# Kernel optimization log

Hardware: AMD Instinct MI355X
Metric: run time of the kernel (lower is better)

The kernel has to match this reference:

```python
import jax, jax.numpy as jnp
import numpy as np

B, L, H = 32, 1024, 512
NEG_INF = -1e30

def setup_inputs() -> dict:
    key = jax.random.key(0)
    k1, k2, k3, k4, k5 = jax.random.split(key, 5)
    c = jax.random.normal(k1, (B, L, H), dtype=jnp.float32)
    c_mask = jax.random.randint(k2, (B, L), 0, 2, dtype=jnp.int32)
    # xavier_uniform-like init scale for [H,1]: sqrt(6/(H+1))
    lim = float(np.sqrt(6.0 / (H + 1)))
    c_weight = jax.random.uniform(k3, (H, 1), minval=-lim, maxval=lim, dtype=jnp.float32)
    q_weight = jax.random.uniform(k4, (H, 1), minval=-lim, maxval=lim, dtype=jnp.float32)
    cq_weight = jax.random.uniform(k5, (1, 1, H), minval=-lim, maxval=lim, dtype=jnp.float32)
    bias = jnp.zeros((1,), dtype=jnp.float32)
    return {"c": c, "c_mask": c_mask, "c_weight": c_weight, "q_weight": q_weight,
            "cq_weight": cq_weight, "bias": bias}

def reference(c, c_mask, c_weight, q_weight, cq_weight, bias):
    m = c_mask.astype(jnp.float32)                     # [B,L]
    # similarity matrix (BiDAF trilinear decomposition), q == c here
    s0 = c @ c_weight                                  # [B,L,1]
    s1 = jnp.swapaxes(c @ q_weight, 1, 2)              # [B,1,L]
    s2 = jnp.einsum('blh,bmh->blm', c * cq_weight, c)  # [B,L,L]
    s = s0 + s1 + s2 + bias                            # [B,L,L]
    mask_row = m[:, None, :]                           # mask over dim=2 (keys)
    mask_col = m[:, :, None]                           # mask over dim=1
    s1p = jax.nn.softmax(mask_row * s + (1.0 - mask_row) * NEG_INF, axis=2)
    s2p = jax.nn.softmax(mask_col * s + (1.0 - mask_col) * NEG_INF, axis=1)
    a = s1p @ c                                        # [B,L,H]
    b = (s1p @ jnp.swapaxes(s2p, 1, 2)) @ c            # [B,L,H]
    return jnp.concatenate([c, a, c * a, c * b], axis=2)  # [B,L,4H]
```

## Files before the change

### kernel.cpp

```cpp
#include <hip/hip_runtime.h>
#include <hip/hip_bf16.h>
#include <stdint.h>

constexpr int Bb = 32;
constexpr int Ll = 1024;
constexpr int Hh = 512;

typedef __attribute__((ext_vector_type(8))) short short8;
typedef __attribute__((ext_vector_type(4))) short short4v;
typedef __attribute__((ext_vector_type(4))) float float4v;
typedef __attribute__((ext_vector_type(4))) int int4v;

__device__ inline short f2bf(float f) {
  union { float f; uint32_t u; } v; v.f = f;
  uint32_t r = (v.u + 0x7FFF + ((v.u >> 16) & 1)) >> 16;
  return (short)r;
}

#define MFMA(a, b, c) __builtin_amdgcn_mfma_f32_16x16x32_bf16(a, b, c, 0, 0, 0)

__device__ inline void gl_lds(const short* g, short* l) {
  __builtin_amdgcn_global_load_lds(
      (const __attribute__((address_space(1))) unsigned int*)g,
      (__attribute__((address_space(3))) unsigned int*)l, 16, 0, 0);
}

template <int ROWS>
__device__ inline void stage(short* lds, const short* g, int sk, int t) {
  const int w = t >> 6;
  const int kbg = (t & 7) ^ ((t >> 3) & 7);
#pragma unroll
  for (int r = 0; r < ROWS / 32; ++r) {
    int row = r * 32 + (t >> 3);
    gl_lds(g + (size_t)row * sk + kbg * 8, lds + (r * 32 + w * 8) * 64);
  }
}

__device__ inline short8 fld(const short* lds, int row, int kb) {
  return *(const short8*)(lds + row * 64 + ((kb ^ (row & 7)) << 3));
}

__global__ __launch_bounds__(256) void k_rowdots(
    const float* __restrict__ c, const float* __restrict__ cw,
    const float* __restrict__ qw, float* __restrict__ s0, float* __restrict__ s1) {
  int row = blockIdx.x * 4 + (threadIdx.x >> 6);
  int lane = threadIdx.x & 63;
  const float* cr = c + (size_t)row * Hh;
  float d0 = 0.f, d1 = 0.f;
#pragma unroll
  for (int i = 0; i < Hh / 64; ++i) {
    int h = lane + i * 64;
    float v = cr[h];
    d0 = fmaf(v, cw[h], d0);
    d1 = fmaf(v, qw[h], d1);
  }
#pragma unroll
  for (int off = 32; off > 0; off >>= 1) {
    d0 += __shfl_down(d0, off);
    d1 += __shfl_down(d1, off);
  }
  if (lane == 0) { s0[row] = d0; s1[row] = d1; }
}

__global__ __launch_bounds__(256) void k_cvt(
    const float* __restrict__ c, const float* __restrict__ cq,
    short* __restrict__ c16, short* __restrict__ cbq16) {
  size_t i8 = ((size_t)blockIdx.x * 256 + threadIdx.x) * 8;
  int h = (int)(i8 & (Hh - 1));
  float4v v0 = *(const float4v*)&c[i8];
  float4v v1 = *(const float4v*)&c[i8 + 4];
  float4v q0 = *(const float4v*)&cq[h];
  float4v q1 = *(const float4v*)&cq[h + 4];
  short8 a, bq;
#pragma unroll
  for (int j = 0; j < 4; ++j) {
    a[j] = f2bf(v0[j]);     a[4 + j] = f2bf(v1[j]);
    bq[j] = f2bf(v0[j] * q0[j]); bq[4 + j] = f2bf(v1[j] * q1[j]);
  }
  *(short8*)&c16[i8] = a;
  *(short8*)&cbq16[i8] = bq;
}

__global__ __launch_bounds__(256) void k_ct(const float* __restrict__ c,
                                            short* __restrict__ cT) {
  const int b = blockIdx.z, h0 = blockIdx.x * 64, l0 = blockIdx.y * 64;
  __shared__ short T[64 * 65];
  const int t = threadIdx.x, rl = t >> 4, c4 = (t & 15) * 4;
#pragma unroll
  for (int p = 0; p < 4; ++p) {
    int ll = rl + p * 16;
    float4v v = *(const float4v*)&c[((size_t)(b * Ll + l0 + ll)) * Hh + h0 + c4];
#pragma unroll
    for (int j = 0; j < 4; ++j) T[ll * 65 + c4 + j] = f2bf(v[j]);
  }
  __syncthreads();
#pragma unroll
  for (int p = 0; p < 4; ++p) {
    int hh = rl + p * 16;
    short4v o;
#pragma unroll
    for (int j = 0; j < 4; ++j) o[j] = T[(c4 + j) * 65 + hh];
    *(short4v*)&cT[((size_t)(b * Hh + h0 + hh)) * Ll + l0 + c4] = o;
  }
}

__global__ __launch_bounds__(256) void k_sgemm(
    const short* __restrict__ Aq, const short* __restrict__ Bc,
    const float* __restrict__ s0, const float* __restrict__ s1,
    const float* __restrict__ bias, float* __restrict__ S) {
  const int b = blockIdx.z, l0 = blockIdx.y * 128, m0 = blockIdx.x * 128;
  __shared__ __align__(16) short As[128 * 64];
  __shared__ __align__(16) short Bs[128 * 64];
  const int t = threadIdx.x, li = t & 63, w = t >> 6;
  const int wy = w >> 1, wx = w & 1, rr = li & 15, q = li >> 4;
  const short* Ag = Aq + ((size_t)b * Ll + l0) * Hh;
  const short* Bg = Bc + ((size_t)b * Ll + m0) * Hh;
  float4v acc[4][4];
#pragma unroll
  for (int i = 0; i < 4; ++i)
#pragma unroll
    for (int j = 0; j < 4; ++j) acc[i][j] = (float4v){0.f, 0.f, 0.f, 0.f};
  for (int kk = 0; kk < Hh; kk += 64) {
    stage<128>(As, Ag + kk, Hh, t);
    stage<128>(Bs, Bg + kk, Hh, t);
    __syncthreads();
#pragma unroll
    for (int ks = 0; ks < 2; ++ks) {
      int kb = ks * 4 + q;
      short8 af[4], bf4[4];
#pragma unroll
      for (int mt = 0; mt < 4; ++mt) af[mt] = fld(As, wy * 64 + mt * 16 + rr, kb);
#pragma unroll
      for (int nt = 0; nt < 4; ++nt) bf4[nt] = fld(Bs, wx * 64 + nt * 16 + rr, kb);
#pragma unroll
      for (int mt = 0; mt < 4; ++mt)
#pragma unroll
        for (int nt = 0; nt < 4; ++nt)
          acc[mt][nt] = MFMA(af[mt], bf4[nt], acc[mt][nt]);
    }
    __syncthreads();
  }
  const float bsc = bias[0];
  float* Sb = S + (size_t)b * Ll * Ll;
#pragma unroll
  for (int nt = 0; nt < 4; ++nt) {
    int m = m0 + wx * 64 + nt * 16 + rr;
    float s1v = s1[b * Ll + m] + bsc;
#pragma unroll
    for (int mt = 0; mt < 4; ++mt) {
#pragma unroll
      for (int i = 0; i < 4; ++i) {
        int l = l0 + wy * 64 + mt * 16 + q * 4 + i;
        Sb[(size_t)l * Ll + m] = acc[mt][nt][i] + s0[b * Ll + l] + s1v;
      }
    }
  }
}

__global__ __launch_bounds__(256) void k_rowstats(
    const float* __restrict__ S, const int* __restrict__ c_mask,
    float* __restrict__ rowmax, float* __restrict__ rowrcp) {
  int row = blockIdx.x * 4 + (threadIdx.x >> 6);
  int b = row >> 10;
  int lane = threadIdx.x & 63;
  const float* Sr = S + (size_t)row * Ll;
  const int* mk = c_mask + b * Ll;
  float vals[16];
  float mx = -INFINITY;
#pragma unroll
  for (int i = 0; i < 16; ++i) {
    int m = lane + i * 64;
    float v = mk[m] ? Sr[m] : -INFINITY;
    vals[i] = v;
    mx = fmaxf(mx, v);
  }
#pragma unroll
  for (int off = 32; off > 0; off >>= 1) mx = fmaxf(mx, __shfl_down(mx, off));
  mx = __shfl(mx, 0);
  float sum = 0.f;
#pragma unroll
  for (int i = 0; i < 16; ++i) sum += __expf(vals[i] - mx);
#pragma unroll
  for (int off = 32; off > 0; off >>= 1) sum += __shfl_down(sum, off);
  if (lane == 0) { rowmax[row] = mx; rowrcp[row] = 1.f / sum; }
}

__global__ __launch_bounds__(256) void k_colpart(
    const float* __restrict__ S, const int* __restrict__ c_mask,
    float* __restrict__ pmax, float* __restrict__ psum) {
  int b = blockIdx.z, l0 = blockIdx.y * 128;
  int m = blockIdx.x * 256 + threadIdx.x;
  const float* Sb = S + (size_t)b * Ll * Ll;
  const int* mk = c_mask + b * Ll;
  float mx = -INFINITY;
  for (int l = l0; l < l0 + 128; ++l)
    if (mk[l]) mx = fmaxf(mx, Sb[(size_t)l * Ll + m]);
  float sum = 0.f;
  if (mx > -INFINITY)
    for (int l = l0; l < l0 + 128; ++l)
      if (mk[l]) sum += __expf(Sb[(size_t)l * Ll + m] - mx);
  int o = blockIdx.y * (Bb * Ll) + b * Ll + m;
  pmax[o] = mx;
  psum[o] = sum;
}

__global__ __launch_bounds__(256) void k_colcomb(
    const float* __restrict__ pmax, const float* __restrict__ psum,
    float* __restrict__ colmax, float* __restrict__ colrcp) {
  int i = blockIdx.x * 256 + threadIdx.x;
  float M = -INFINITY;
#pragma unroll
  for (int k = 0; k < 8; ++k) M = fmaxf(M, pmax[k * (Bb * Ll) + i]);
  float s = 0.f;
#pragma unroll
  for (int k = 0; k < 8; ++k) {
    float pm = pmax[k * (Bb * Ll) + i];
    if (pm > -INFINITY) s += psum[k * (Bb * Ll) + i] * __expf(pm - M);
  }
  colmax[i] = M;
  colrcp[i] = 1.f / s;
}

__global__ __launch_bounds__(256) void k_p1(
    const float* __restrict__ S, const int* __restrict__ c_mask,
    const float* __restrict__ rowmax, const float* __restrict__ rowrcp,
    short* __restrict__ P1) {
  size_t gi = (size_t)blockIdx.x * 256 + threadIdx.x;
  size_t idx = gi * 8;
  int row = (int)(gi >> 7);
  int b = row >> 10;
  int m = ((int)gi & 127) * 8;
  float rm = rowmax[row], rr = rowrcp[row];
  int4v k0 = *(const int4v*)&c_mask[b * Ll + m];
  int4v k1 = *(const int4v*)&c_mask[b * Ll + m + 4];
  float4v v0 = *(const float4v*)&S[idx];
  float4v v1 = *(const float4v*)&S[idx + 4];
  short8 o;
#pragma unroll
  for (int j = 0; j < 4; ++j) {
    o[j] = k0[j] ? f2bf(__expf(v0[j] - rm) * rr) : (short)0;
    o[4 + j] = k1[j] ? f2bf(__expf(v1[j] - rm) * rr) : (short)0;
  }
  *(short8*)&P1[idx] = o;
}

__global__ __launch_bounds__(256) void k_p2t(
    const float* __restrict__ S, const int* __restrict__ c_mask,
    const float* __restrict__ colmax, const float* __restrict__ colrcp,
    short* __restrict__ P2T) {
  const int b = blockIdx.z, m0 = blockIdx.x * 64, l0 = blockIdx.y * 64;
  __shared__ short T[64 * 65];
  const int t = threadIdx.x, rl = t >> 4, c4 = (t & 15) * 4;
  const float* Sb = S + (size_t)b * Ll * Ll;
  float4v cm = *(const float4v*)&colmax[b * Ll + m0 + c4];
  float4v cr = *(const float4v*)&colrcp[b * Ll + m0 + c4];
#pragma unroll
  for (int p = 0; p < 4; ++p) {
    int ll = rl + p * 16;
    int mk = c_mask[b * Ll + l0 + ll];
    float4v v = *(const float4v*)&Sb[(size_t)(l0 + ll) * Ll + m0 + c4];
#pragma unroll
    for (int j = 0; j < 4; ++j)
      T[ll * 65 + c4 + j] = mk ? f2bf(__expf(v[j] - cm[j]) * cr[j]) : (short)0;
  }
  __syncthreads();
#pragma unroll
  for (int p = 0; p < 4; ++p) {
    int mm = rl + p * 16;
    short4v o;
#pragma unroll
    for (int j = 0; j < 4; ++j) o[j] = T[(c4 + j) * 65 + mm];
    *(short4v*)&P2T[((size_t)(b * Ll + m0 + mm)) * Ll + l0 + c4] = o;
  }
}

__global__ __launch_bounds__(256) void k_ugemm(
    const short* __restrict__ P2T, const short* __restrict__ cT,
    short* __restrict__ uT) {
  const int b = blockIdx.z, m0 = blockIdx.y * 128, h0 = blockIdx.x * 128;
  __shared__ __align__(16) short As[128 * 64];
  __shared__ __align__(16) short Bs[128 * 64];
  const int t = threadIdx.x, li = t & 63, w = t >> 6;
  const int wy = w >> 1, wx = w & 1, rr = li & 15, q = li >> 4;
  const short* Ag = P2T + ((size_t)b * Ll + m0) * Ll;
  const short* Bg = cT + ((size_t)b * Hh + h0) * Ll;
  float4v acc[4][4];
#pragma unroll
  for (int i = 0; i < 4; ++i)
#pragma unroll
    for (int j = 0; j < 4; ++j) acc[i][j] = (float4v){0.f, 0.f, 0.f, 0.f};
  for (int kk = 0; kk < Ll; kk += 64) {
    stage<128>(As, Ag + kk, Ll, t);
    stage<128>(Bs, Bg + kk, Ll, t);
    __syncthreads();
#pragma unroll
    for (int ks = 0; ks < 2; ++ks) {
      int kb = ks * 4 + q;
      short8 af[4], bf4[4];
#pragma unroll
      for (int mt = 0; mt < 4; ++mt) af[mt] = fld(As, wy * 64 + mt * 16 + rr, kb);
#pragma unroll
      for (int nt = 0; nt < 4; ++nt) bf4[nt] = fld(Bs, wx * 64 + nt * 16 + rr, kb);
#pragma unroll
      for (int mt = 0; mt < 4; ++mt)
#pragma unroll
        for (int nt = 0; nt < 4; ++nt)
          acc[mt][nt] = MFMA(af[mt], bf4[nt], acc[mt][nt]);
    }
    __syncthreads();
  }
#pragma unroll
  for (int nt = 0; nt < 4; ++nt) {
    int h = h0 + wx * 64 + nt * 16 + rr;
#pragma unroll
    for (int mt = 0; mt < 4; ++mt) {
      int mb = m0 + wy * 64 + mt * 16 + q * 4;
      short4v o;
#pragma unroll
      for (int i = 0; i < 4; ++i) o[i] = f2bf(acc[mt][nt][i]);
      *(short4v*)&uT[((size_t)b * Hh + h) * Ll + mb] = o;
    }
  }
}

__global__ __launch_bounds__(256) void k_abgemm(
    const short* __restrict__ P1, const short* __restrict__ cT,
    const short* __restrict__ uT, const float* __restrict__ c,
    float* __restrict__ out) {
  const int b = blockIdx.z, l0 = blockIdx.y * 128, h0 = blockIdx.x * 64;
  __shared__ __align__(16) short As[128 * 64];
  __shared__ __align__(16) short B1s[64 * 64];
  __shared__ __align__(16) short B2s[64 * 64];
  const int t = threadIdx.x, li = t & 63, w = t >> 6;
  const int wy = w >> 1, wx = w & 1, rr = li & 15, q = li >> 4;
  const short* Ag = P1 + ((size_t)b * Ll + l0) * Ll;
  const short* B1g = cT + ((size_t)b * Hh + h0) * Ll;
  const short* B2g = uT + ((size_t)b * Hh + h0) * Ll;
  float4v aa[4][2], ab[4][2];
#pragma unroll
  for (int i = 0; i < 4; ++i)
#pragma unroll
    for (int j = 0; j < 2; ++j) {
      aa[i][j] = (float4v){0.f, 0.f, 0.f, 0.f};
      ab[i][j] = (float4v){0.f, 0.f, 0.f, 0.f};
    }
  for (int kk = 0; kk < Ll; kk += 64) {
    stage<128>(As, Ag + kk, Ll, t);
    stage<64>(B1s, B1g + kk, Ll, t);
    stage<64>(B2s, B2g + kk, Ll, t);
    __syncthreads();
#pragma unroll
    for (int ks = 0; ks < 2; ++ks) {
      int kb = ks * 4 + q;
      short8 af[4], b1[2], b2[2];
#pragma unroll
      for (int mt = 0; mt < 4; ++mt) af[mt] = fld(As, wy * 64 + mt * 16 + rr, kb);
#pragma unroll
      for (int nt = 0; nt < 2; ++nt) {
        b1[nt] = fld(B1s, wx * 32 + nt * 16 + rr, kb);
        b2[nt] = fld(B2s, wx * 32 + nt * 16 + rr, kb);
      }
#pragma unroll
      for (int mt = 0; mt < 4; ++mt)
#pragma unroll
        for (int nt = 0; nt < 2; ++nt) {
          aa[mt][nt] = MFMA(af[mt], b1[nt], aa[mt][nt]);
          ab[mt][nt] = MFMA(af[mt], b2[nt], ab[mt][nt]);
        }
    }
    __syncthreads();
  }
#pragma unroll
  for (int nt = 0; nt < 2; ++nt) {
    int h = h0 + wx * 32 + nt * 16 + rr;
#pragma unroll
    for (int mt = 0; mt < 4; ++mt) {
#pragma unroll
      for (int i = 0; i < 4; ++i) {
        int l = l0 + wy * 64 + mt * 16 + q * 4 + i;
        float cv = c[((size_t)b * Ll + l) * Hh + h];
        size_t ob = ((size_t)b * Ll + l) * (size_t)(4 * Hh);
        float av = aa[mt][nt][i], bv = ab[mt][nt][i];
        out[ob + h] = cv;
        out[ob + Hh + h] = av;
        out[ob + 2 * Hh + h] = cv * av;
        out[ob + 3 * Hh + h] = cv * bv;
      }
    }
  }
}

extern "C" void kernel_launch(void* const* d_in, const int* in_sizes, int n_in,
                              void* d_out, int out_size, void* d_ws, size_t ws_size,
                              hipStream_t stream) {
  const float* c = (const float*)d_in[0];
  const int* c_mask = (const int*)d_in[1];
  const float* c_weight = (const float*)d_in[2];
  const float* q_weight = (const float*)d_in[3];
  const float* cq = (const float*)d_in[4];
  const float* bias = (const float*)d_in[5];
  float* out = (float*)d_out;

  char* ws = (char*)d_ws;
  float* S = (float*)ws;
  short* uT = (short*)ws;
  short* cT16 = (short*)(ws + 134217728ull);
  short* c16 = (short*)(ws + 167772160ull);
  short* P1 = (short*)(ws + 167772160ull);
  short* cbq16 = (short*)(ws + 201326592ull);
  short* P2T = (short*)(ws + 234881024ull);
  float* st = (float*)(ws + 301989888ull);
  float* s0 = st;
  float* s1 = st + 32768;
  float* rowmax = st + 65536;
  float* rowrcp = st + 98304;
  float* colmax = st + 131072;
  float* colrcp = st + 163840;
  float* pmax = st + 196608;
  float* psum = st + 458752;

  k_rowdots<<<dim3(Bb * Ll / 4), dim3(256), 0, stream>>>(c, c_weight, q_weight, s0, s1);
  k_cvt<<<dim3(8192), dim3(256), 0, stream>>>(c, cq, c16, cbq16);
  k_ct<<<dim3(Hh / 64, Ll / 64, Bb), dim3(256), 0, stream>>>(c, cT16);
  k_sgemm<<<dim3(Ll / 128, Ll / 128, Bb), dim3(256), 0, stream>>>(cbq16, c16, s0, s1, bias, S);
  k_rowstats<<<dim3(Bb * Ll / 4), dim3(256), 0, stream>>>(S, c_mask, rowmax, rowrcp);
  k_colpart<<<dim3(Ll / 256, 8, Bb), dim3(256), 0, stream>>>(S, c_mask, pmax, psum);
  k_colcomb<<<dim3(Bb * Ll / 256), dim3(256), 0, stream>>>(pmax, psum, colmax, colrcp);
  k_p1<<<dim3(16384), dim3(256), 0, stream>>>(S, c_mask, rowmax, rowrcp, P1);
  k_p2t<<<dim3(Ll / 64, Ll / 64, Bb), dim3(256), 0, stream>>>(S, c_mask, colmax, colrcp, P2T);
  k_ugemm<<<dim3(Hh / 128, Ll / 128, Bb), dim3(256), 0, stream>>>(P2T, cT16, uT);
  k_abgemm<<<dim3(Hh / 64, Ll / 128, Bb), dim3(256), 0, stream>>>(P1, cT16, uT, c, out);
}
```

Measured before the change: 850.9 us.

## Fuse softmax partial stats into S GEMM epilogue and merge P1/P2T passes

The S GEMM epilogue now computes per-tile row and column partial max and sum-exp using shuffles and LDS reductions. This replaces the separate rowstats and colpart kernels, which each reread the full 128MB S matrix. P1 and P2T are now produced in one kernel that reads S once, and block indices are remapped across the three GEMMs, likely to improve L2/XCD locality. abgemm gets an occupancy hint. The cost is a heavier GEMM epilogue with extra syncs and register pressure.

Result: faster. 688.9 us (-19.0%).

```diff
diff --git a/kernel.cpp b/kernel.cpp
--- a/kernel.cpp
+++ b/kernel.cpp
@@ -107,8 +107,13 @@
 __global__ __launch_bounds__(256) void k_sgemm(
     const short* __restrict__ Aq, const short* __restrict__ Bc,
     const float* __restrict__ s0, const float* __restrict__ s1,
-    const float* __restrict__ bias, float* __restrict__ S) {
-  const int b = blockIdx.z, l0 = blockIdx.y * 128, m0 = blockIdx.x * 128;
+    const float* __restrict__ bias, const int* __restrict__ c_mask,
+    float* __restrict__ S,
+    float* __restrict__ rowpmax, float* __restrict__ rowpsum,
+    float* __restrict__ colpmax, float* __restrict__ colpsum) {
+  int flat = blockIdx.x + ((blockIdx.y + (blockIdx.z << 3)) << 3);
+  flat = ((flat & 7) << 8) | (flat >> 3);
+  const int b = flat >> 6, l0 = ((flat >> 3) & 7) << 7, m0 = (flat & 7) << 7;
   __shared__ __align__(16) short As[128 * 64];
   __shared__ __align__(16) short Bs[128 * 64];
   const int t = threadIdx.x, li = t & 63, w = t >> 6;
@@ -141,72 +146,143 @@
     __syncthreads();
   }
   const float bsc = bias[0];
+  float s1v[4]; int mkm[4];
+#pragma unroll
+  for (int nt = 0; nt < 4; ++nt) {
+    int m = m0 + wx * 64 + nt * 16 + rr;
+    s1v[nt] = s1[b * Ll + m] + bsc;
+    mkm[nt] = c_mask[b * Ll + m];
+  }
+  int mkl[4][4];
+#pragma unroll
+  for (int mt = 0; mt < 4; ++mt)
+#pragma unroll
+    for (int i = 0; i < 4; ++i) {
+      int l = l0 + wy * 64 + mt * 16 + q * 4 + i;
+      float s0v = s0[b * Ll + l];
+      mkl[mt][i] = c_mask[b * Ll + l];
+#pragma unroll
+      for (int nt = 0; nt < 4; ++nt) acc[mt][nt][i] += s0v + s1v[nt];
+    }
   float* Sb = S + (size_t)b * Ll * Ll;
 #pragma unroll
   for (int nt = 0; nt < 4; ++nt) {
     int m = m0 + wx * 64 + nt * 16 + rr;
-    float s1v = s1[b * Ll + m] + bsc;
-#pragma unroll
-    for (int mt = 0; mt < 4; ++mt) {
+#pragma unroll
+    for (int mt = 0; mt < 4; ++mt)
 #pragma unroll
       for (int i = 0; i < 4; ++i) {
         int l = l0 + wy * 64 + mt * 16 + q * 4 + i;
-        Sb[(size_t)l * Ll + m] = acc[mt][nt][i] + s0[b * Ll + l] + s1v;
+        Sb[(size_t)l * Ll + m] = acc[mt][nt][i];
       }
-    }
-  }
-}
-
-__global__ __launch_bounds__(256) void k_rowstats(
-    const float* __restrict__ S, const int* __restrict__ c_mask,
-    float* __restrict__ rowmax, float* __restrict__ rowrcp) {
-  int row = blockIdx.x * 4 + (threadIdx.x >> 6);
-  int b = row >> 10;
-  int lane = threadIdx.x & 63;
-  const float* Sr = S + (size_t)row * Ll;
-  const int* mk = c_mask + b * Ll;
-  float vals[16];
-  float mx = -INFINITY;
-#pragma unroll
-  for (int i = 0; i < 16; ++i) {
-    int m = lane + i * 64;
-    float v = mk[m] ? Sr[m] : -INFINITY;
-    vals[i] = v;
-    mx = fmaxf(mx, v);
-  }
-#pragma unroll
-  for (int off = 32; off > 0; off >>= 1) mx = fmaxf(mx, __shfl_down(mx, off));
-  mx = __shfl(mx, 0);
-  float sum = 0.f;
-#pragma unroll
-  for (int i = 0; i < 16; ++i) sum += __expf(vals[i] - mx);
-#pragma unroll
-  for (int off = 32; off > 0; off >>= 1) sum += __shfl_down(sum, off);
-  if (lane == 0) { rowmax[row] = mx; rowrcp[row] = 1.f / sum; }
-}
-
-__global__ __launch_bounds__(256) void k_colpart(
-    const float* __restrict__ S, const int* __restrict__ c_mask,
-    float* __restrict__ pmax, float* __restrict__ psum) {
-  int b = blockIdx.z, l0 = blockIdx.y * 128;
-  int m = blockIdx.x * 256 + threadIdx.x;
-  const float* Sb = S + (size_t)b * Ll * Ll;
-  const int* mk = c_mask + b * Ll;
-  float mx = -INFINITY;
-  for (int l = l0; l < l0 + 128; ++l)
-    if (mk[l]) mx = fmaxf(mx, Sb[(size_t)l * Ll + m]);
-  float sum = 0.f;
-  if (mx > -INFINITY)
-    for (int l = l0; l < l0 + 128; ++l)
-      if (mk[l]) sum += __expf(Sb[(size_t)l * Ll + m] - mx);
-  int o = blockIdx.y * (Bb * Ll) + b * Ll + m;
-  pmax[o] = mx;
-  psum[o] = sum;
-}
-
-__global__ __launch_bounds__(256) void k_colcomb(
+  }
+  float* red = (float*)As;
+  const size_t rbase = (size_t)(m0 >> 7) * (Bb * Ll) + (size_t)b * Ll + l0;
+  const size_t cbase = (size_t)(l0 >> 7) * (Bb * Ll) + (size_t)b * Ll + m0;
+  float rv[16];
+#pragma unroll
+  for (int mt = 0; mt < 4; ++mt)
+#pragma unroll
+    for (int i = 0; i < 4; ++i) {
+      float v = -INFINITY;
+#pragma unroll
+      for (int nt = 0; nt < 4; ++nt) v = mkm[nt] ? fmaxf(v, acc[mt][nt][i]) : v;
+      rv[mt * 4 + i] = v;
+    }
+#pragma unroll
+  for (int off = 1; off < 16; off <<= 1)
+#pragma unroll
+    for (int j = 0; j < 16; ++j) rv[j] = fmaxf(rv[j], __shfl_xor(rv[j], off));
+  if (rr == 0)
+#pragma unroll
+    for (int j = 0; j < 16; ++j)
+      red[wx * 128 + wy * 64 + (j >> 2) * 16 + q * 4 + (j & 3)] = rv[j];
+  __syncthreads();
+  if (t < 128) {
+    float M = fmaxf(red[t], red[128 + t]);
+    red[t] = M;
+    rowpmax[rbase + t] = M;
+  }
+  __syncthreads();
+#pragma unroll
+  for (int mt = 0; mt < 4; ++mt)
+#pragma unroll
+    for (int i = 0; i < 4; ++i) {
+      float M = red[wy * 64 + mt * 16 + q * 4 + i];
+      float sacc = 0.f;
+      if (M > -INFINITY) {
+#pragma unroll
+        for (int nt = 0; nt < 4; ++nt)
+          sacc += mkm[nt] ? __expf(acc[mt][nt][i] - M) : 0.f;
+      }
+      rv[mt * 4 + i] = sacc;
+    }
+#pragma unroll
+  for (int off = 1; off < 16; off <<= 1)
+#pragma unroll
+    for (int j = 0; j < 16; ++j) rv[j] += __shfl_xor(rv[j], off);
+  __syncthreads();
+  if (rr == 0)
+#pragma unroll
+    for (int j = 0; j < 16; ++j)
+      red[wx * 128 + wy * 64 + (j >> 2) * 16 + q * 4 + (j & 3)] = rv[j];
+  __syncthreads();
+  if (t < 128) rowpsum[rbase + t] = red[t] + red[128 + t];
+  float cv[4];
+#pragma unroll
+  for (int nt = 0; nt < 4; ++nt) {
+    float v = -INFINITY;
+#pragma unroll
+    for (int mt = 0; mt < 4; ++mt)
+#pragma unroll
+      for (int i = 0; i < 4; ++i) v = mkl[mt][i] ? fmaxf(v, acc[mt][nt][i]) : v;
+    cv[nt] = v;
+  }
+#pragma unroll
+  for (int nt = 0; nt < 4; ++nt) {
+    cv[nt] = fmaxf(cv[nt], __shfl_xor(cv[nt], 16));
+    cv[nt] = fmaxf(cv[nt], __shfl_xor(cv[nt], 32));
+  }
+  __syncthreads();
+  if (q == 0)
+#pragma unroll
+    for (int nt = 0; nt < 4; ++nt) red[wy * 128 + wx * 64 + nt * 16 + rr] = cv[nt];
+  __syncthreads();
+  if (t < 128) {
+    float M = fmaxf(red[t], red[128 + t]);
+    red[t] = M;
+    colpmax[cbase + t] = M;
+  }
+  __syncthreads();
+#pragma unroll
+  for (int nt = 0; nt < 4; ++nt) {
+    float M = red[wx * 64 + nt * 16 + rr];
+    float sacc = 0.f;
+    if (M > -INFINITY) {
+#pragma unroll
+      for (int mt = 0; mt < 4; ++mt)
+#pragma unroll
+        for (int i = 0; i < 4; ++i)
+          sacc += mkl[mt][i] ? __expf(acc[mt][nt][i] - M) : 0.f;
+    }
+    cv[nt] = sacc;
+  }
+#pragma unroll
+  for (int nt = 0; nt < 4; ++nt) {
+    cv[nt] += __shfl_xor(cv[nt], 16);
+    cv[nt] += __shfl_xor(cv[nt], 32);
+  }
+  __syncthreads();
+  if (q == 0)
+#pragma unroll
+    for (int nt = 0; nt < 4; ++nt) red[wy * 128 + wx * 64 + nt * 16 + rr] = cv[nt];
+  __syncthreads();
+  if (t < 128) colpsum[cbase + t] = red[t] + red[128 + t];
+}
+
+__global__ __launch_bounds__(256) void k_comb(
     const float* __restrict__ pmax, const float* __restrict__ psum,
-    float* __restrict__ colmax, float* __restrict__ colrcp) {
+    float* __restrict__ omax, float* __restrict__ orcp) {
   int i = blockIdx.x * 256 + threadIdx.x;
   float M = -INFINITY;
 #pragma unroll
@@ -217,51 +293,36 @@
     float pm = pmax[k * (Bb * Ll) + i];
     if (pm > -INFINITY) s += psum[k * (Bb * Ll) + i] * __expf(pm - M);
   }
-  colmax[i] = M;
-  colrcp[i] = 1.f / s;
-}
-
-__global__ __launch_bounds__(256) void k_p1(
+  omax[i] = M;
+  orcp[i] = 1.f / s;
+}
+
+__global__ __launch_bounds__(256) void k_p12(
     const float* __restrict__ S, const int* __restrict__ c_mask,
     const float* __restrict__ rowmax, const float* __restrict__ rowrcp,
-    short* __restrict__ P1) {
-  size_t gi = (size_t)blockIdx.x * 256 + threadIdx.x;
-  size_t idx = gi * 8;
-  int row = (int)(gi >> 7);
-  int b = row >> 10;
-  int m = ((int)gi & 127) * 8;
-  float rm = rowmax[row], rr = rowrcp[row];
-  int4v k0 = *(const int4v*)&c_mask[b * Ll + m];
-  int4v k1 = *(const int4v*)&c_mask[b * Ll + m + 4];
-  float4v v0 = *(const float4v*)&S[idx];
-  float4v v1 = *(const float4v*)&S[idx + 4];
-  short8 o;
-#pragma unroll
-  for (int j = 0; j < 4; ++j) {
-    o[j] = k0[j] ? f2bf(__expf(v0[j] - rm) * rr) : (short)0;
-    o[4 + j] = k1[j] ? f2bf(__expf(v1[j] - rm) * rr) : (short)0;
-  }
-  *(short8*)&P1[idx] = o;
-}
-
-__global__ __launch_bounds__(256) void k_p2t(
-    const float* __restrict__ S, const int* __restrict__ c_mask,
     const float* __restrict__ colmax, const float* __restrict__ colrcp,
-    short* __restrict__ P2T) {
+    short* __restrict__ P1, short* __restrict__ P2T) {
   const int b = blockIdx.z, m0 = blockIdx.x * 64, l0 = blockIdx.y * 64;
   __shared__ short T[64 * 65];
   const int t = threadIdx.x, rl = t >> 4, c4 = (t & 15) * 4;
   const float* Sb = S + (size_t)b * Ll * Ll;
   float4v cm = *(const float4v*)&colmax[b * Ll + m0 + c4];
   float4v cr = *(const float4v*)&colrcp[b * Ll + m0 + c4];
+  int4v mkm = *(const int4v*)&c_mask[b * Ll + m0 + c4];
 #pragma unroll
   for (int p = 0; p < 4; ++p) {
     int ll = rl + p * 16;
-    int mk = c_mask[b * Ll + l0 + ll];
+    int gl = b * Ll + l0 + ll;
+    int mkl = c_mask[gl];
+    float rm = rowmax[gl], rrc = rowrcp[gl];
     float4v v = *(const float4v*)&Sb[(size_t)(l0 + ll) * Ll + m0 + c4];
-#pragma unroll
-    for (int j = 0; j < 4; ++j)
-      T[ll * 65 + c4 + j] = mk ? f2bf(__expf(v[j] - cm[j]) * cr[j]) : (short)0;
+    short4v o1;
+#pragma unroll
+    for (int j = 0; j < 4; ++j) {
+      o1[j] = mkm[j] ? f2bf(__expf(v[j] - rm) * rrc) : (short)0;
+      T[ll * 65 + c4 + j] = mkl ? f2bf(__expf(v[j] - cm[j]) * cr[j]) : (short)0;
+    }
+    *(short4v*)&P1[(size_t)gl * Ll + m0 + c4] = o1;
   }
   __syncthreads();
 #pragma unroll
@@ -277,7 +338,9 @@
 __global__ __launch_bounds__(256) void k_ugemm(
     const short* __restrict__ P2T, const short* __restrict__ cT,
     short* __restrict__ uT) {
-  const int b = blockIdx.z, m0 = blockIdx.y * 128, h0 = blockIdx.x * 128;
+  int flat = blockIdx.x + ((blockIdx.y + (blockIdx.z << 3)) << 2);
+  flat = ((flat & 7) << 7) | (flat >> 3);
+  const int b = flat >> 5, m0 = ((flat >> 2) & 7) << 7, h0 = (flat & 3) << 7;
   __shared__ __align__(16) short As[128 * 64];
   __shared__ __align__(16) short Bs[128 * 64];
   const int t = threadIdx.x, li = t & 63, w = t >> 6;
@@ -323,11 +386,13 @@
   }
 }
 
-__global__ __launch_bounds__(256) void k_abgemm(
+__global__ __launch_bounds__(256, 4) void k_abgemm(
     const short* __restrict__ P1, const short* __restrict__ cT,
     const short* __restrict__ uT, const float* __restrict__ c,
     float* __restrict__ out) {
-  const int b = blockIdx.z, l0 = blockIdx.y * 128, h0 = blockIdx.x * 64;
+  int flat = blockIdx.x + ((blockIdx.y + (blockIdx.z << 3)) << 3);
+  flat = ((flat & 7) << 8) | (flat >> 3);
+  const int b = flat >> 6, l0 = ((flat >> 3) & 7) << 7, h0 = (flat & 7) << 6;
   __shared__ __align__(16) short As[128 * 64];
   __shared__ __align__(16) short B1s[64 * 64];
   __shared__ __align__(16) short B2s[64 * 64];
@@ -409,6 +474,10 @@
   short* P1 = (short*)(ws + 167772160ull);
   short* cbq16 = (short*)(ws + 201326592ull);
   short* P2T = (short*)(ws + 234881024ull);
+  float* rowpmax = (float*)(ws + 234881024ull);
+  float* rowpsum = (float*)(ws + 234881024ull + 1048576ull);
+  float* colpmax = (float*)(ws + 234881024ull + 2097152ull);
+  float* colpsum = (float*)(ws + 234881024ull + 3145728ull);
   float* st = (float*)(ws + 301989888ull);
   float* s0 = st;
   float* s1 = st + 32768;
@@ -416,18 +485,16 @@
   float* rowrcp = st + 98304;
   float* colmax = st + 131072;
   float* colrcp = st + 163840;
-  float* pmax = st + 196608;
-  float* psum = st + 458752;
 
   k_rowdots<<<dim3(Bb * Ll / 4), dim3(256), 0, stream>>>(c, c_weight, q_weight, s0, s1);
   k_cvt<<<dim3(8192), dim3(256), 0, stream>>>(c, cq, c16, cbq16);
   k_ct<<<dim3(Hh / 64, Ll / 64, Bb), dim3(256), 0, stream>>>(c, cT16);
-  k_sgemm<<<dim3(Ll / 128, Ll / 128, Bb), dim3(256), 0, stream>>>(cbq16, c16, s0, s1, bias, S);
-  k_rowstats<<<dim3(Bb * Ll / 4), dim3(256), 0, stream>>>(S, c_mask, rowmax, rowrcp);
-  k_colpart<<<dim3(Ll / 256, 8, Bb), dim3(256), 0, stream>>>(S, c_mask, pmax, psum);
-  k_colcomb<<<dim3(Bb * Ll / 256), dim3(256), 0, stream>>>(pmax, psum, colmax, colrcp);
-  k_p1<<<dim3(16384), dim3(256), 0, stream>>>(S, c_mask, rowmax, rowrcp, P1);
-  k_p2t<<<dim3(Ll / 64, Ll / 64, Bb), dim3(256), 0, stream>>>(S, c_mask, colmax, colrcp, P2T);
+  k_sgemm<<<dim3(Ll / 128, Ll / 128, Bb), dim3(256), 0, stream>>>(
+      cbq16, c16, s0, s1, bias, c_mask, S, rowpmax, rowpsum, colpmax, colpsum);
+  k_comb<<<dim3(Bb * Ll / 256), dim3(256), 0, stream>>>(rowpmax, rowpsum, rowmax, rowrcp);
+  k_comb<<<dim3(Bb * Ll / 256), dim3(256), 0, stream>>>(colpmax, colpsum, colmax, colrcp);
+  k_p12<<<dim3(Ll / 64, Ll / 64, Bb), dim3(256), 0, stream>>>(
+      S, c_mask, rowmax, rowrcp, colmax, colrcp, P1, P2T);
   k_ugemm<<<dim3(Hh / 128, Ll / 128, Bb), dim3(256), 0, stream>>>(P2T, cT16, uT);
   k_abgemm<<<dim3(Hh / 64, Ll / 128, Bb), dim3(256), 0, stream>>>(P1, cT16, uT, c, out);
 }
```
